# Performance work log

Measured on AMD Instinct MI355X. Metric: run time of the kernel, lower is better.

## Reference

```python
import jax, jax.numpy as jnp
import numpy as np

N_SPK, N_UTT, D = 512, 64, 1024
EPS = 1e-6  # matches tf.math.l2_normalize default epsilon guard


def _l2norm(x, axis=-1):
    return x / jnp.sqrt(jnp.maximum(jnp.sum(x * x, axis=axis, keepdims=True), EPS))


def setup_inputs() -> dict:
    key = jax.random.key(0)
    k1, _ = jax.random.split(key)
    inputs = jax.random.normal(k1, (N_SPK, N_UTT, D), dtype=jnp.float32)
    w = jnp.asarray(10.0, dtype=jnp.float32)
    b = jnp.asarray(-5.0, dtype=jnp.float32)
    return {"inputs": inputs, "w": w, "b": b}


def reference(inputs, w, b):
    N, M, _ = inputs.shape
    # speaker centroids: mean over utterances -> [N, D]
    centroids = jnp.mean(inputs, axis=1)
    # utterance (exclusion) centroids: mean of the other M-1 utterances -> [N, M, D]
    ut_centroids = (jnp.sum(inputs, axis=1, keepdims=True) - inputs) / (M - 1)

    e = _l2norm(inputs)          # [N, M, D]
    c = _l2norm(centroids)       # [N, D]
    uc = _l2norm(ut_centroids)   # [N, M, D]

    # cosine sim of every utterance vs every speaker centroid -> [N, M, K]
    cos_all = jnp.einsum('nmd,kd->nmk', e, c)
    # same-speaker entries use the self-exclusion centroid
    cos_self = jnp.sum(e * uc, axis=-1)  # [N, M]
    eye = jnp.eye(N, dtype=inputs.dtype)[:, None, :]  # [N, 1, N]
    cos_sim = cos_all * (1.0 - eye) + cos_self[:, :, None] * eye

    sim = w * cos_sim + b  # [N, M, N]
    # softmax contrastive loss: -S_{j,i,j} + logsumexp_k S_{j,i,k}, summed
    lse = jax.nn.logsumexp(sim, axis=-1)            # [N, M]
    pos = jnp.einsum('nmn->nm', sim)                # diagonal along speaker axes
    loss = jnp.sum(lse - pos)
    return loss
```

## Files before the change

kernel.cpp:

```cpp
#include <hip/hip_runtime.h>
#include <stdint.h>

#define N_SPK 512
#define N_UTT 64
#define DIM   1024
#define NROWS (N_SPK * N_UTT)
#define EPS   1e-6f

#define BM2 256
#define BN2 256
#define BK2 32
#define KT2 (DIM / BK2)

typedef __attribute__((ext_vector_type(8))) short short8;
typedef __attribute__((ext_vector_type(4))) float f32x4;

__device__ __forceinline__ uint16_t f2bf(float f) {
    union { float f; uint32_t i; } un; un.f = f;
    uint32_t x = un.i;
    return (uint16_t)((x + 0x7fffu + ((x >> 16) & 1u)) >> 16);
}

__global__ __launch_bounds__(256) void prep_centroid(
    const float* __restrict__ x, uint16_t* __restrict__ xb,
    uint16_t* __restrict__ cmat, float* __restrict__ xxg,
    float* __restrict__ ssqg)
{
    const int n    = blockIdx.x;
    const int tid  = threadIdx.x;
    const int lane = tid & 63;
    const int w    = tid >> 6;

    const float* xn  = x  + (size_t)n * N_UTT * DIM;
    uint16_t*    xbn = xb + (size_t)n * N_UTT * DIM;

    float Sp[16];
    #pragma unroll
    for (int j = 0; j < 16; ++j) Sp[j] = 0.f;

    #pragma unroll 1
    for (int o = 0; o < 4; ++o) {
        const int m0 = w * 16 + o * 4;

        float4 v[16];
        #pragma unroll
        for (int i = 0; i < 4; ++i)
            #pragma unroll
            for (int j = 0; j < 4; ++j)
                v[i * 4 + j] = *(const float4*)(xn + (size_t)(m0 + i) * DIM + j * 256 + lane * 4);

        float xx[4] = {0.f, 0.f, 0.f, 0.f};
        #pragma unroll
        for (int i = 0; i < 4; ++i) {
            #pragma unroll
            for (int j = 0; j < 4; ++j) {
                const float4 qv = v[i * 4 + j];
                xx[i] += qv.x * qv.x + qv.y * qv.y + qv.z * qv.z + qv.w * qv.w;
                Sp[j * 4 + 0] += qv.x; Sp[j * 4 + 1] += qv.y;
                Sp[j * 4 + 2] += qv.z; Sp[j * 4 + 3] += qv.w;
                ushort4 ov;
                ov.x = f2bf(qv.x); ov.y = f2bf(qv.y); ov.z = f2bf(qv.z); ov.w = f2bf(qv.w);
                *(ushort4*)(xbn + (size_t)(m0 + i) * DIM + j * 256 + lane * 4) = ov;
            }
        }

        #pragma unroll
        for (int i = 0; i < 4; ++i) {
            float t = xx[i];
            #pragma unroll
            for (int off = 1; off < 64; off <<= 1) t += __shfl_xor(t, off);
            if (lane == 0) xxg[n * N_UTT + m0 + i] = t;
        }
    }

    __shared__ float Sh[4][DIM];
    #pragma unroll
    for (int j = 0; j < 4; ++j)
        *(float4*)&Sh[w][j * 256 + lane * 4] =
            make_float4(Sp[j * 4], Sp[j * 4 + 1], Sp[j * 4 + 2], Sp[j * 4 + 3]);
    __syncthreads();

    const int d0 = tid * 4;
    float4 S  = *(const float4*)&Sh[0][d0];
    const float4 b1 = *(const float4*)&Sh[1][d0];
    const float4 b2 = *(const float4*)&Sh[2][d0];
    const float4 b3 = *(const float4*)&Sh[3][d0];
    S.x += b1.x + b2.x + b3.x; S.y += b1.y + b2.y + b3.y;
    S.z += b1.z + b2.z + b3.z; S.w += b1.w + b2.w + b3.w;

    float css = S.x * S.x + S.y * S.y + S.z * S.z + S.w * S.w;
    #pragma unroll
    for (int off = 1; off < 64; off <<= 1) css += __shfl_xor(css, off);
    __shared__ float red[4];
    if ((tid & 63) == 0) red[tid >> 6] = css;
    __syncthreads();
    const float ssq = red[0] + red[1] + red[2] + red[3];

    const float scale = rsqrtf(fmaxf(ssq * (1.0f / 4096.f), EPS)) * (1.0f / 64.f);
    ushort4 oc;
    oc.x = f2bf(S.x * scale); oc.y = f2bf(S.y * scale);
    oc.z = f2bf(S.z * scale); oc.w = f2bf(S.w * scale);
    *(ushort4*)(cmat + (size_t)n * DIM + d0) = oc;
    if (tid == 0) ssqg[n] = ssq;
}

__global__ __launch_bounds__(512, 2) void gemm_lse_kernel(
    const uint16_t* __restrict__ xb, const uint16_t* __restrict__ cmat,
    const float* __restrict__ xxg, const float* __restrict__ ssqg,
    const float* __restrict__ wp, const float* __restrict__ bp,
    float* __restrict__ sumexp2, float* __restrict__ pos)
{
    __shared__ char smem[98304];
    float* Se = (float*)smem;

    const int tid   = threadIdx.x;
    const int lane  = tid & 63;
    const int wid   = tid >> 6;
    const int waveM = wid >> 2;
    const int waveN = wid & 3;

    const int bid = blockIdx.x;
    const int rt  = bid & 127;
    const int ct  = bid >> 7;

    const int rowBase = rt * BM2;
    const int colBase = ct * BN2;

    const uint16_t* gAp[2];
    const uint16_t* gBp[2];
    int ldso[2];
    #pragma unroll
    for (int i = 0; i < 2; ++i) {
        const int s    = i * 512 + tid;
        const int srow = s >> 2;
        const int kc   = (s & 3) ^ ((srow >> 1) & 3);
        gAp[i]  = xb   + (size_t)(rowBase + srow) * DIM + kc * 8;
        gBp[i]  = cmat + (size_t)(colBase + srow) * DIM + kc * 8;
        ldso[i] = s * 16;
    }

#define STAGE(slot, kt_)                                                        \
    {                                                                           \
        const int ko_ = (kt_) * BK2;                                            \
        _Pragma("unroll")                                                       \
        for (int i_ = 0; i_ < 2; ++i_) {                                        \
            __builtin_amdgcn_global_load_lds(                                   \
                (const __attribute__((address_space(1))) void*)(gAp[i_] + ko_), \
                (__attribute__((address_space(3))) void*)(smem + (slot) * 16384 + ldso[i_]), \
                16, 0, 0);                                                      \
            __builtin_amdgcn_global_load_lds(                                   \
                (const __attribute__((address_space(1))) void*)(gBp[i_] + ko_), \
                (__attribute__((address_space(3))) void*)(smem + 49152 + (slot) * 16384 + ldso[i_]), \
                16, 0, 0);                                                      \
        }                                                                       \
    }

    f32x4 acc[8][4];
    #pragma unroll
    for (int i = 0; i < 8; ++i)
        #pragma unroll
        for (int j = 0; j < 4; ++j)
            acc[i][j] = (f32x4){0.f, 0.f, 0.f, 0.f};

    const int cL  = lane & 15;
    const int q   = lane >> 4;
    const int kcs = q ^ ((cL >> 1) & 3);

#define COMPUTE(slot_)                                                          \
    {                                                                           \
        const uint16_t* Ab_ = (const uint16_t*)(smem + (slot_) * 16384);        \
        const uint16_t* Bb_ = (const uint16_t*)(smem + 49152 + (slot_) * 16384);\
        short8 a_[8], b_[4];                                                    \
        _Pragma("unroll")                                                       \
        for (int bi_ = 0; bi_ < 8; ++bi_)                                       \
            a_[bi_] = *(const short8*)&Ab_[(waveM * 128 + bi_ * 16 + cL) * 32 + kcs * 8]; \
        _Pragma("unroll")                                                       \
        for (int bj_ = 0; bj_ < 4; ++bj_)                                       \
            b_[bj_] = *(const short8*)&Bb_[(waveN * 64 + bj_ * 16 + cL) * 32 + kcs * 8]; \
        __builtin_amdgcn_s_setprio(1);                                          \
        _Pragma("unroll")                                                       \
        for (int bi_ = 0; bi_ < 8; ++bi_)                                       \
            _Pragma("unroll")                                                   \
            for (int bj_ = 0; bj_ < 4; ++bj_)                                   \
                acc[bi_][bj_] = __builtin_amdgcn_mfma_f32_16x16x32_bf16(        \
                    a_[bi_], b_[bj_], acc[bi_][bj_], 0, 0, 0);                  \
        __builtin_amdgcn_s_setprio(0);                                          \
    }

#define ITER(kt_, cSlot, sSlot)                                                 \
    {                                                                           \
        asm volatile("s_waitcnt vmcnt(4)" ::: "memory");                        \
        __builtin_amdgcn_sched_barrier(0);                                      \
        __builtin_amdgcn_s_barrier();                                           \
        __builtin_amdgcn_sched_barrier(0);                                      \
        STAGE(sSlot, (kt_) + 2);                                                \
        COMPUTE(cSlot);                                                         \
    }

    STAGE(0, 0);
    STAGE(1, 1);

    for (int tb = 0; tb < 30; tb += 3) {
        ITER(tb + 0, 0, 2);
        ITER(tb + 1, 1, 0);
        ITER(tb + 2, 2, 1);
    }
    asm volatile("s_waitcnt vmcnt(4)" ::: "memory");
    __builtin_amdgcn_sched_barrier(0);
    __builtin_amdgcn_s_barrier();
    __builtin_amdgcn_sched_barrier(0);
    COMPUTE(0);
    asm volatile("s_waitcnt vmcnt(0)" ::: "memory");
    __builtin_amdgcn_sched_barrier(0);
    __builtin_amdgcn_s_barrier();
    __builtin_amdgcn_sched_barrier(0);
    COMPUTE(1);
#undef STAGE
#undef COMPUTE
#undef ITER

    __syncthreads();
    const float wv = wp[0], bv = bp[0];
    #pragma unroll
    for (int bi = 0; bi < 8; ++bi) {
        #pragma unroll
        for (int r = 0; r < 4; ++r) {
            const int R     = rowBase + waveM * 128 + bi * 16 + q * 4 + r;
            const float xxv = xxg[R];
            const float rn  = rsqrtf(fmaxf(xxv, EPS));
            const int nrow  = R >> 6;
            float s = 0.f;
            #pragma unroll
            for (int bj = 0; bj < 4; ++bj) {
                const int col = colBase + waveN * 64 + bj * 16 + cL;
                const float dot = acc[bi][bj][r];
                float sim;
                if (col == nrow) {
                    const float ssqv = ssqg[nrow];
                    const float xs   = dot * sqrtf(ssqv);
                    const float d2   = ssqv - 2.f * xs + xxv;
                    const float cs   = ((xs - xxv) * (1.f / 63.f)) * rn *
                                       rsqrtf(fmaxf(d2 * (1.f / 3969.f), EPS));
                    sim = wv * cs + bv;
                    pos[R] = sim;
                } else {
                    sim = wv * (dot * rn) + bv;
                }
                s += __expf(sim);
            }
            #pragma unroll
            for (int off = 1; off < 16; off <<= 1) s += __shfl_xor(s, off);
            if (cL == 0)
                Se[waveN * 256 + waveM * 128 + bi * 16 + q * 4 + r] = s;
        }
    }
    __syncthreads();
    if (tid < 256) {
        const float t = Se[tid] + Se[256 + tid] + Se[512 + tid] + Se[768 + tid];
        sumexp2[(size_t)ct * NROWS + rowBase + tid] = t;
    }
}

__global__ __launch_bounds__(256) void finalize_part(
    const float* __restrict__ pos, const float* __restrict__ se2,
    float* __restrict__ partial)
{
    const int tid = threadIdx.x;
    const int r   = blockIdx.x * 256 + tid;
    const float s = se2[r] + se2[NROWS + r];
    float acc = __logf(s) - pos[r];
    #pragma unroll
    for (int off = 1; off < 64; off <<= 1) acc += __shfl_xor(acc, off);
    __shared__ float red[4];
    if ((tid & 63) == 0) red[tid >> 6] = acc;
    __syncthreads();
    if (tid == 0) partial[blockIdx.x] = red[0] + red[1] + red[2] + red[3];
}

__global__ __launch_bounds__(128) void finalize_sum(
    const float* __restrict__ partial, float* __restrict__ out)
{
    const int tid = threadIdx.x;
    float t = partial[tid];
    #pragma unroll
    for (int off = 1; off < 64; off <<= 1) t += __shfl_xor(t, off);
    __shared__ float red[2];
    if ((tid & 63) == 0) red[tid >> 6] = t;
    __syncthreads();
    if (tid == 0) out[0] = red[0] + red[1];
}

extern "C" void kernel_launch(void* const* d_in, const int* in_sizes, int n_in,
                              void* d_out, int out_size, void* d_ws, size_t ws_size,
                              hipStream_t stream)
{
    const float* x  = (const float*)d_in[0];
    const float* wp = (const float*)d_in[1];
    const float* bp = (const float*)d_in[2];
    float* out = (float*)d_out;

    char* ws = (char*)d_ws;
    size_t off = 0;
    uint16_t* xb      = (uint16_t*)(ws + off); off += (size_t)NROWS * DIM * 2;
    uint16_t* cmat    = (uint16_t*)(ws + off); off += (size_t)N_SPK * DIM * 2;
    float*    xxg     = (float*)(ws + off);    off += (size_t)NROWS * 4;
    float*    pos     = (float*)(ws + off);    off += (size_t)NROWS * 4;
    float*    sumexp2 = (float*)(ws + off);    off += (size_t)2 * NROWS * 4;
    float*    ssqg    = (float*)(ws + off);    off += (size_t)N_SPK * 4;
    float*    partial = (float*)(ws + off);    off += (size_t)128 * 4;

    prep_centroid<<<N_SPK, 256, 0, stream>>>(x, xb, cmat, xxg, ssqg);
    gemm_lse_kernel<<<(NROWS / BM2) * (N_SPK / BN2), 512, 0, stream>>>(
        xb, cmat, xxg, ssqg, wp, bp, sumexp2, pos);
    finalize_part<<<NROWS / 256, 256, 0, stream>>>(pos, sumexp2, partial);
    finalize_sum<<<1, 128, 0, stream>>>(partial, out);
}
```

Measured before the change: 250.8 us.

## Use full-width column tiles so each block finishes logsumexp and drops finalize pass

The GEMM tile changes from 256x256 to 128x512, so each block covers all 512 speaker centroids for its rows. The full row log-sum-exp and the positive term can then be computed inside the block, which removes the sumexp/pos global buffers and the finalize_part kernel launch. The cost is one block per CU (larger LDS footprint, more B loads per stage), and the centroid matrix is re-read by every block.

```diff
diff --git a/kernel.cpp b/kernel.cpp
--- a/kernel.cpp
+++ b/kernel.cpp
@@ -7,10 +7,11 @@
 #define NROWS (N_SPK * N_UTT)
 #define EPS   1e-6f
 
-#define BM2 256
-#define BN2 256
-#define BK2 32
-#define KT2 (DIM / BK2)
+#define BMF 128
+#define BNF 512
+#define BKF 32
+#define KTF (DIM / BKF)
+#define SLOT_BYTES 40960
 
 typedef __attribute__((ext_vector_type(8))) short short8;
 typedef __attribute__((ext_vector_type(4))) float f32x4;
@@ -104,14 +105,13 @@
     if (tid == 0) ssqg[n] = ssq;
 }
 
-__global__ __launch_bounds__(512, 2) void gemm_lse_kernel(
+__global__ __launch_bounds__(512, 1) void gemm_lse_kernel(
     const uint16_t* __restrict__ xb, const uint16_t* __restrict__ cmat,
     const float* __restrict__ xxg, const float* __restrict__ ssqg,
     const float* __restrict__ wp, const float* __restrict__ bp,
-    float* __restrict__ sumexp2, float* __restrict__ pos)
-{
-    __shared__ char smem[98304];
-    float* Se = (float*)smem;
+    float* __restrict__ partial)
+{
+    __shared__ char smem[3 * SLOT_BYTES];
 
     const int tid   = threadIdx.x;
     const int lane  = tid & 63;
@@ -119,47 +119,38 @@
     const int waveM = wid >> 2;
     const int waveN = wid & 3;
 
-    const int bid = blockIdx.x;
-    const int rt  = bid & 127;
-    const int ct  = bid >> 7;
-
-    const int rowBase = rt * BM2;
-    const int colBase = ct * BN2;
-
-    const uint16_t* gAp[2];
-    const uint16_t* gBp[2];
-    int ldso[2];
-    #pragma unroll
-    for (int i = 0; i < 2; ++i) {
-        const int s    = i * 512 + tid;
-        const int srow = s >> 2;
-        const int kc   = (s & 3) ^ ((srow >> 1) & 3);
-        gAp[i]  = xb   + (size_t)(rowBase + srow) * DIM + kc * 8;
-        gBp[i]  = cmat + (size_t)(colBase + srow) * DIM + kc * 8;
-        ldso[i] = s * 16;
+    const int rowBase = blockIdx.x * BMF;
+
+    const uint16_t* gsrc[5];
+    int ldso[5];
+    {
+        const int srow = tid >> 2;
+        const int kc   = (tid & 3) ^ ((srow >> 1) & 3);
+        gsrc[0] = xb + (size_t)(rowBase + srow) * DIM + kc * 8;
+        ldso[0] = tid * 16;
+    }
+    #pragma unroll
+    for (int i = 1; i < 5; ++i) {
+        const int s    = tid + (i - 1) * 512;
+        const int brow = s >> 2;
+        const int kc   = (s & 3) ^ ((brow >> 1) & 3);
+        gsrc[i] = cmat + (size_t)brow * DIM + kc * 8;
+        ldso[i] = 8192 + s * 16;
     }
 
 #define STAGE(slot, kt_)                                                        \
-    {                                                                           \
-        const int ko_ = (kt_) * BK2;                                            \
-        _Pragma("unroll")                                                       \
-        for (int i_ = 0; i_ < 2; ++i_) {                                        \
-            __builtin_amdgcn_global_load_lds(                                   \
-                (const __attribute__((address_space(1))) void*)(gAp[i_] + ko_), \
-                (__attribute__((address_space(3))) void*)(smem + (slot) * 16384 + ldso[i_]), \
-                16, 0, 0);                                                      \
-            __builtin_amdgcn_global_load_lds(                                   \
-                (const __attribute__((address_space(1))) void*)(gBp[i_] + ko_), \
-                (__attribute__((address_space(3))) void*)(smem + 49152 + (slot) * 16384 + ldso[i_]), \
-                16, 0, 0);                                                      \
-        }                                                                       \
-    }
-
-    f32x4 acc[8][4];
-    #pragma unroll
-    for (int i = 0; i < 8; ++i)
-        #pragma unroll
-        for (int j = 0; j < 4; ++j)
+    { _Pragma("unroll")                                                         \
+      for (int i_ = 0; i_ < 5; ++i_) {                                          \
+        __builtin_amdgcn_global_load_lds(                                       \
+            (const __attribute__((address_space(1))) void*)(gsrc[i_] + (kt_) * BKF), \
+            (__attribute__((address_space(3))) void*)(smem + (slot) * SLOT_BYTES + ldso[i_]), \
+            16, 0, 0); } }
+
+    f32x4 acc[4][8];
+    #pragma unroll
+    for (int i = 0; i < 4; ++i)
+        #pragma unroll
+        for (int j = 0; j < 8; ++j)
             acc[i][j] = (f32x4){0.f, 0.f, 0.f, 0.f};
 
     const int cL  = lane & 15;
@@ -168,20 +159,20 @@
 
 #define COMPUTE(slot_)                                                          \
     {                                                                           \
-        const uint16_t* Ab_ = (const uint16_t*)(smem + (slot_) * 16384);        \
-        const uint16_t* Bb_ = (const uint16_t*)(smem + 49152 + (slot_) * 16384);\
-        short8 a_[8], b_[4];                                                    \
+        const char* Ab_ = smem + (slot_) * SLOT_BYTES;                          \
+        const char* Bb_ = smem + (slot_) * SLOT_BYTES + 8192;                   \
+        short8 a_[4], b_[8];                                                    \
         _Pragma("unroll")                                                       \
-        for (int bi_ = 0; bi_ < 8; ++bi_)                                       \
-            a_[bi_] = *(const short8*)&Ab_[(waveM * 128 + bi_ * 16 + cL) * 32 + kcs * 8]; \
+        for (int bi_ = 0; bi_ < 4; ++bi_)                                       \
+            a_[bi_] = *(const short8*)(Ab_ + (waveM * 64 + bi_ * 16 + cL) * 64 + kcs * 16); \
         _Pragma("unroll")                                                       \
-        for (int bj_ = 0; bj_ < 4; ++bj_)                                       \
-            b_[bj_] = *(const short8*)&Bb_[(waveN * 64 + bj_ * 16 + cL) * 32 + kcs * 8]; \
+        for (int bj_ = 0; bj_ < 8; ++bj_)                                       \
+            b_[bj_] = *(const short8*)(Bb_ + (waveN * 128 + bj_ * 16 + cL) * 64 + kcs * 16); \
         __builtin_amdgcn_s_setprio(1);                                          \
         _Pragma("unroll")                                                       \
-        for (int bi_ = 0; bi_ < 8; ++bi_)                                       \
+        for (int bi_ = 0; bi_ < 4; ++bi_)                                       \
             _Pragma("unroll")                                                   \
-            for (int bj_ = 0; bj_ < 4; ++bj_)                                   \
+            for (int bj_ = 0; bj_ < 8; ++bj_)                                   \
                 acc[bi_][bj_] = __builtin_amdgcn_mfma_f32_16x16x32_bf16(        \
                     a_[bi_], b_[bj_], acc[bi_][bj_], 0, 0, 0);                  \
         __builtin_amdgcn_s_setprio(0);                                          \
@@ -189,7 +180,7 @@
 
 #define ITER(kt_, cSlot, sSlot)                                                 \
     {                                                                           \
-        asm volatile("s_waitcnt vmcnt(4)" ::: "memory");                        \
+        asm volatile("s_waitcnt vmcnt(5)" ::: "memory");                        \
         __builtin_amdgcn_sched_barrier(0);                                      \
         __builtin_amdgcn_s_barrier();                                           \
         __builtin_amdgcn_sched_barrier(0);                                      \
@@ -205,7 +196,7 @@
         ITER(tb + 1, 1, 0);
         ITER(tb + 2, 2, 1);
     }
-    asm volatile("s_waitcnt vmcnt(4)" ::: "memory");
+    asm volatile("s_waitcnt vmcnt(5)" ::: "memory");
     __builtin_amdgcn_sched_barrier(0);
     __builtin_amdgcn_s_barrier();
     __builtin_amdgcn_sched_barrier(0);
@@ -220,19 +211,24 @@
 #undef ITER
 
     __syncthreads();
+    float* Se  = (float*)smem;
+    float* Pe  = (float*)(smem + 2048);
+    float* red = (float*)(smem + 2560);
+
     const float wv = wp[0], bv = bp[0];
     #pragma unroll
-    for (int bi = 0; bi < 8; ++bi) {
+    for (int bi = 0; bi < 4; ++bi) {
         #pragma unroll
         for (int r = 0; r < 4; ++r) {
-            const int R     = rowBase + waveM * 128 + bi * 16 + q * 4 + r;
+            const int lr    = waveM * 64 + bi * 16 + q * 4 + r;
+            const int R     = rowBase + lr;
             const float xxv = xxg[R];
             const float rn  = rsqrtf(fmaxf(xxv, EPS));
             const int nrow  = R >> 6;
             float s = 0.f;
             #pragma unroll
-            for (int bj = 0; bj < 4; ++bj) {
-                const int col = colBase + waveN * 64 + bj * 16 + cL;
+            for (int bj = 0; bj < 8; ++bj) {
+                const int col = waveN * 128 + bj * 16 + cL;
                 const float dot = acc[bi][bj][r];
                 float sim;
                 if (col == nrow) {
@@ -242,7 +238,7 @@
                     const float cs   = ((xs - xxv) * (1.f / 63.f)) * rn *
                                        rsqrtf(fmaxf(d2 * (1.f / 3969.f), EPS));
                     sim = wv * cs + bv;
-                    pos[R] = sim;
+                    Pe[lr] = sim;
                 } else {
                     sim = wv * (dot * rn) + bv;
                 }
@@ -250,44 +246,32 @@
             }
             #pragma unroll
             for (int off = 1; off < 16; off <<= 1) s += __shfl_xor(s, off);
-            if (cL == 0)
-                Se[waveN * 256 + waveM * 128 + bi * 16 + q * 4 + r] = s;
+            if (cL == 0) Se[waveN * 128 + lr] = s;
         }
     }
     __syncthreads();
-    if (tid < 256) {
-        const float t = Se[tid] + Se[256 + tid] + Se[512 + tid] + Se[768 + tid];
-        sumexp2[(size_t)ct * NROWS + rowBase + tid] = t;
-    }
-}
-
-__global__ __launch_bounds__(256) void finalize_part(
-    const float* __restrict__ pos, const float* __restrict__ se2,
-    float* __restrict__ partial)
-{
-    const int tid = threadIdx.x;
-    const int r   = blockIdx.x * 256 + tid;
-    const float s = se2[r] + se2[NROWS + r];
-    float acc = __logf(s) - pos[r];
-    #pragma unroll
-    for (int off = 1; off < 64; off <<= 1) acc += __shfl_xor(acc, off);
-    __shared__ float red[4];
-    if ((tid & 63) == 0) red[tid >> 6] = acc;
-    __syncthreads();
-    if (tid == 0) partial[blockIdx.x] = red[0] + red[1] + red[2] + red[3];
-}
-
-__global__ __launch_bounds__(128) void finalize_sum(
+    if (tid < 128) {
+        const float tot = Se[tid] + Se[128 + tid] + Se[256 + tid] + Se[384 + tid];
+        float lt = __logf(tot) - Pe[tid];
+        #pragma unroll
+        for (int off = 1; off < 64; off <<= 1) lt += __shfl_xor(lt, off);
+        if ((tid & 63) == 0) red[tid >> 6] = lt;
+    }
+    __syncthreads();
+    if (tid == 0) partial[blockIdx.x] = red[0] + red[1];
+}
+
+__global__ __launch_bounds__(256) void finalize_sum(
     const float* __restrict__ partial, float* __restrict__ out)
 {
     const int tid = threadIdx.x;
     float t = partial[tid];
     #pragma unroll
     for (int off = 1; off < 64; off <<= 1) t += __shfl_xor(t, off);
-    __shared__ float red[2];
+    __shared__ float red[4];
     if ((tid & 63) == 0) red[tid >> 6] = t;
     __syncthreads();
-    if (tid == 0) out[0] = red[0] + red[1];
+    if (tid == 0) out[0] = red[0] + red[1] + red[2] + red[3];
 }
 
 extern "C" void kernel_launch(void* const* d_in, const int* in_sizes, int n_in,
@@ -304,14 +288,11 @@
     uint16_t* xb      = (uint16_t*)(ws + off); off += (size_t)NROWS * DIM * 2;
     uint16_t* cmat    = (uint16_t*)(ws + off); off += (size_t)N_SPK * DIM * 2;
     float*    xxg     = (float*)(ws + off);    off += (size_t)NROWS * 4;
-    float*    pos     = (float*)(ws + off);    off += (size_t)NROWS * 4;
-    float*    sumexp2 = (float*)(ws + off);    off += (size_t)2 * NROWS * 4;
     float*    ssqg    = (float*)(ws + off);    off += (size_t)N_SPK * 4;
-    float*    partial = (float*)(ws + off);    off += (size_t)128 * 4;
+    float*    partial = (float*)(ws + off);    off += (size_t)256 * 4;
 
     prep_centroid<<<N_SPK, 256, 0, stream>>>(x, xb, cmat, xxg, ssqg);
-    gemm_lse_kernel<<<(NROWS / BM2) * (N_SPK / BN2), 512, 0, stream>>>(
-        xb, cmat, xxg, ssqg, wp, bp, sumexp2, pos);
-    finalize_part<<<NROWS / 256, 256, 0, stream>>>(pos, sumexp2, partial);
-    finalize_sum<<<1, 128, 0, stream>>>(partial, out);
-}
+    gemm_lse_kernel<<<NROWS / BMF, 512, 0, stream>>>(
+        xb, cmat, xxg, ssqg, wp, bp, partial);
+    finalize_sum<<<1, 256, 0, stream>>>(partial, out);
+}
```

Result: faster. 244.2 us (median of 2 runs) (-2.6%).
